# Kernel tuning notes

Measured on AMD Instinct MI355X. Metric: run time of the kernel, lower is better.

Reference implementation:

```python
import jax, jax.numpy as jnp
import numpy as np
from jax import lax

B, T, D, K = 2, 4096, 128, 256


def setup_inputs() -> dict:
    key = jax.random.key(0)
    ks = jax.random.split(key, 5)
    s = 0.05
    return {
        "z": jax.random.normal(ks[0], (B, T, D), jnp.float32),
        "conv_kernel": jax.random.normal(ks[1], (K, 1, D), jnp.float32) * s,  # flax WIO depthwise
        "conv_bias": jnp.zeros((D,), jnp.float32),
        "Wq": jax.random.normal(ks[2], (D, D), jnp.float32) * s,
        "bq": jnp.zeros((D,), jnp.float32),
        "Wk": jax.random.normal(ks[3], (D, D), jnp.float32) * s,
        "bk": jnp.zeros((D,), jnp.float32),
        "Wo": jax.random.normal(ks[4], (D, D), jnp.float32) * s,
        "bo": jnp.zeros((D,), jnp.float32),
    }


def _sphere_norm(x):
    return x / jnp.maximum(jnp.linalg.norm(x, axis=-1, keepdims=True), 1e-8)


def reference(z, conv_kernel, conv_bias, Wq, bq, Wk, bk, Wo, bo):
    Bv, Tv, Dv = z.shape
    Kv = conv_kernel.shape[0]

    # Depthwise causal memory conv (flax nn.Conv, padding='CAUSAL', groups=D)
    memory_force = lax.conv_general_dilated(
        z, conv_kernel, window_strides=(1,), padding=[(Kv - 1, 0)],
        dimension_numbers=("NWC", "WIO", "NWC"), feature_group_count=Dv,
    ) + conv_bias

    # Keys are computed from the base point z once, shared across RK4 stages
    k_hat = _sphere_norm(z @ Wk + bk)  # [B,T,D]
    mask = jnp.tril(jnp.ones((Tv, Tv), z.dtype))  # causal mask

    def vector_field(z_curr):
        q_hat = _sphere_norm(z_curr @ Wq + bq)
        dots = jnp.einsum("btd,bsd->bts", q_hat, k_hat)  # [B,T,T]
        attn = jnp.sin(dots) * mask  # Kuramoto-style sin coupling, causal
        kuramoto = jnp.einsum("bts,bsd->btd", attn, k_hat) @ Wo + bo
        total = memory_force + kuramoto
        # project to tangent space of the sphere at z_curr
        return total - jnp.sum(total * z_curr, axis=-1, keepdims=True) * z_curr

    h = 1.0

    def retract(z_base, v):
        return _sphere_norm(z_base + v)

    k1 = vector_field(z)
    k2 = vector_field(retract(z, 0.5 * h * k1))
    k3 = vector_field(retract(z, 0.5 * h * k2))
    k4 = vector_field(retract(z, h * k3))
    v_final = (h / 6.0) * (k1 + 2 * k2 + 2 * k3 + k4)
    return retract(z, v_final)
```

## Files before the change

kernel.cpp:

```cpp
#include <hip/hip_runtime.h>
#include <hip/hip_bf16.h>

#define BB 2
#define TT 4096
#define DD 128
#define KK 256
#define NROW (BB*TT)
#define NELT (NROW*DD)

typedef _Float16 f16;
typedef __attribute__((ext_vector_type(8))) f16 half8;
typedef __attribute__((ext_vector_type(2))) __fp16 fp16x2;
typedef __attribute__((ext_vector_type(4))) float f32x4;
typedef __attribute__((ext_vector_type(2))) int i32x2;

__device__ __forceinline__ int pack2(float a, float b){
  fp16x2 h = __builtin_amdgcn_cvt_pkrtz(a, b);
  return __builtin_bit_cast(int, h);
}

__device__ __forceinline__ void stage_w_f16(int tid, const float* __restrict__ W, f16* Wh){
  #pragma unroll
  for (int it = 0; it < 8; it++){
    int idx = tid + it*256;
    f32x4 a = *(const f32x4*)(W + (size_t)idx*8);
    f32x4 b = *(const f32x4*)(W + (size_t)idx*8 + 4);
    half8 h;
    #pragma unroll
    for (int u = 0; u < 4; u++){ h[u] = (f16)a[u]; h[4+u] = (f16)b[u]; }
    *(half8*)(Wh + (size_t)idx*8) = h;
  }
}

__device__ __forceinline__ void proj_norm_rows(
    int tid, int r0,
    const float* __restrict__ src, const float* __restrict__ W, const float* __restrict__ bias,
    f16* __restrict__ dst, f16* __restrict__ dstT)
{
  __shared__ f16 Wh[DD*DD];
  __shared__ float zs[32*DD];
  stage_w_f16(tid, W, Wh);
  #pragma unroll
  for (int it = 0; it < 4; it++){
    int idx = tid + it*256;
    *(f32x4*)(zs + idx*4) = *(const f32x4*)(src + (size_t)r0*DD + idx*4);
  }
  __syncthreads();
  int c = tid & 15, rr = tid >> 4;
  float acc0[8], acc1[8];
  #pragma unroll
  for (int u = 0; u < 8; u++){ float bv = bias[c*8+u]; acc0[u] = bv; acc1[u] = bv; }
  const float* zr0 = zs + rr*DD;
  const float* zr1 = zs + (rr+16)*DD;
  #pragma unroll 4
  for (int i = 0; i < DD; i++){
    half8 wv = *(const half8*)(Wh + i*DD + c*8);
    float a0 = zr0[i], a1 = zr1[i];
    #pragma unroll
    for (int u = 0; u < 8; u++){
      float w = (float)wv[u];
      acc0[u] = fmaf(a0, w, acc0[u]);
      acc1[u] = fmaf(a1, w, acc1[u]);
    }
  }
  float s0 = 0.f, s1 = 0.f;
  #pragma unroll
  for (int u = 0; u < 8; u++){ s0 = fmaf(acc0[u], acc0[u], s0); s1 = fmaf(acc1[u], acc1[u], s1); }
  #pragma unroll
  for (int m = 1; m < 16; m <<= 1){ s0 += __shfl_xor(s0, m, 16); s1 += __shfl_xor(s1, m, 16); }
  float inv0 = 1.f / fmaxf(sqrtf(s0), 1e-8f);
  float inv1 = 1.f / fmaxf(sqrtf(s1), 1e-8f);
  half8 h0, h1;
  #pragma unroll
  for (int u = 0; u < 8; u++){ h0[u] = (f16)(acc0[u]*inv0); h1[u] = (f16)(acc1[u]*inv1); }
  int row0 = r0 + rr, row1 = row0 + 16;
  *(half8*)(dst + (size_t)row0*DD + c*8) = h0;
  *(half8*)(dst + (size_t)row1*DD + c*8) = h1;
  if (dstT){
    int b = row0 >> 12, t0 = row0 & 4095, t1 = row1 & 4095;
    #pragma unroll
    for (int u = 0; u < 8; u++){
      dstT[((size_t)b*DD + c*8 + u)*TT + t0] = h0[u];
      dstT[((size_t)b*DD + c*8 + u)*TT + t1] = h1[u];
    }
  }
}

__global__ __launch_bounds__(256) void k_prep(
    const float* __restrict__ z, const float* __restrict__ Wk, const float* __restrict__ bk,
    const float* __restrict__ ck, const float* __restrict__ cb,
    const float* __restrict__ Wq, const float* __restrict__ bq,
    f16* __restrict__ khb, f16* __restrict__ khT, f16* __restrict__ qhb,
    float* __restrict__ mf)
{
  int tid = threadIdx.x;
  if (blockIdx.x < 512){
    int bid = blockIdx.x;
    int d = tid & 127, tg = tid >> 7;
    int b = bid >> 8;
    int tbase = ((bid & 255) << 4) + tg*8;
    const float* zb = z + (size_t)b*TT*DD;
    float acc[8];
    #pragma unroll
    for (int j = 0; j < 8; j++) acc[j] = 0.f;
    float ckq[8];
    #pragma unroll
    for (int u = 0; u < 8; u++) ckq[u] = 0.f;
    int sstart = tbase - (KK-1);
    for (int ch = 0; ch < 33; ch++){
      #pragma unroll
      for (int u = 0; u < 8; u++){
        int base = ch*8 + u;
        int s = sstart + base;
        float zv = ((unsigned)s < (unsigned)TT && base < 263) ? zb[(size_t)s*DD + d] : 0.f;
        ckq[u] = (base < KK) ? ck[(size_t)base*DD + d] : 0.f;
        #pragma unroll
        for (int j = 0; j < 8; j++) acc[j] = fmaf(ckq[(u-j)&7], zv, acc[j]);
      }
    }
    float cbv = cb[d];
    #pragma unroll
    for (int j = 0; j < 8; j++)
      mf[((size_t)b*TT + tbase + j)*DD + d] = acc[j] + cbv;
  } else if (blockIdx.x < 768){
    proj_norm_rows(tid, (blockIdx.x - 512) * 32, z, Wk, bk, khb, khT);
  } else {
    proj_norm_rows(tid, (blockIdx.x - 768) * 32, z, Wq, bq, qhb, nullptr);
  }
}

#define QTILE 128
#define NQT3 (TT/QTILE)
#define NCHUNK 272

__global__ __launch_bounds__(256,2) void k_attn13(
    const f16* __restrict__ qhb, const f16* __restrict__ khb,
    const f16* __restrict__ khT, f16* __restrict__ part)
{
  int bid = blockIdx.x;
  int b = bid / NCHUNK;
  int rem = bid - b*NCHUNK;
  int qt = 0, chunk = 0;
  #pragma unroll 1
  for (int j = NQT3-1; j >= 0; j--){
    int nch = (2*j + 5) >> 2;
    if (rem < nch){ qt = j; chunk = rem; break; }
    rem -= nch;
  }
  int kt0 = chunk * 4;
  int kt1 = min(kt0 + 3, 2*qt + 1);
  int t0 = qt * QTILE;

  __shared__ __align__(16) f16 Kb[64*136];
  __shared__ __align__(16) f16 Kt[128*72];
  __shared__ __align__(16) f16 Ps[4][32*72];

  int tid  = threadIdx.x;
  int w    = tid >> 6;
  int lane = tid & 63;
  int n16  = lane & 15;
  int g    = lane >> 4;

  const f16* qg  = qhb + (size_t)b*TT*DD;
  const f16* kg  = khb + (size_t)b*TT*DD;
  const f16* ktg = khT + (size_t)b*DD*TT;

  int sb_r  = tid >> 4, sb_c = (tid & 15)*8;
  int st_r  = tid >> 3, st_c = (tid & 7)*8;

  half8 qa[2][4];
  #pragma unroll
  for (int p = 0; p < 2; p++){
    const f16* qrow = qg + (size_t)(t0 + 32*w + 16*p + n16)*DD + g*8;
    #pragma unroll
    for (int c = 0; c < 4; c++) qa[p][c] = *(const half8*)(qrow + 32*c);
  }
  f32x4 acc[2][8];
  #pragma unroll
  for (int p = 0; p < 2; p++)
    #pragma unroll
    for (int i = 0; i < 8; i++) acc[p][i] = (f32x4){0.f,0.f,0.f,0.f};

  f16* psw = &Ps[w][0];

  half8 sKb[4], sKt[4];
  {
    int s0 = kt0 * 64;
    #pragma unroll
    for (int it = 0; it < 4; it++)
      sKb[it] = *(const half8*)(kg + (size_t)(s0 + sb_r + it*16)*DD + sb_c);
    #pragma unroll
    for (int it = 0; it < 4; it++)
      sKt[it] = *(const half8*)(ktg + (size_t)(st_r + it*32)*TT + s0 + st_c);
  }

  for (int kt = kt0; kt <= kt1; kt++){
    #pragma unroll
    for (int it = 0; it < 4; it++)
      *(half8*)(Kb + (sb_r + it*16)*136 + sb_c) = sKb[it];
    #pragma unroll
    for (int it = 0; it < 4; it++)
      *(half8*)(Kt + (st_r + it*32)*72 + st_c) = sKt[it];
    __syncthreads();

    if (kt < kt1){
      int s0n = (kt+1) * 64;
      #pragma unroll
      for (int it = 0; it < 4; it++)
        sKb[it] = *(const half8*)(kg + (size_t)(s0n + sb_r + it*16)*DD + sb_c);
      #pragma unroll
      for (int it = 0; it < 4; it++)
        sKt[it] = *(const half8*)(ktg + (size_t)(st_r + it*32)*TT + s0n + st_c);
    }

    int s0 = kt * 64;
    f32x4 s_acc[2][4];
    #pragma unroll
    for (int p = 0; p < 2; p++)
      #pragma unroll
      for (int n = 0; n < 4; n++) s_acc[p][n] = (f32x4){0.f,0.f,0.f,0.f};
    #pragma unroll
    for (int c = 0; c < 4; c++){
      #pragma unroll
      for (int n = 0; n < 4; n++){
        half8 af = *(const half8*)(Kb + (16*n + n16)*136 + 32*c + g*8);
        s_acc[0][n] = __builtin_amdgcn_mfma_f32_16x16x32_f16(af, qa[0][c], s_acc[0][n], 0,0,0);
        s_acc[1][n] = __builtin_amdgcn_mfma_f32_16x16x32_f16(af, qa[1][c], s_acc[1][n], 0,0,0);
      }
    }
    #pragma unroll
    for (int p = 0; p < 2; p++){
      int qrow = t0 + 32*w + 16*p + n16;
      #pragma unroll
      for (int n = 0; n < 4; n++){
        int keyr = s0 + 16*n + 4*g;
        float v0 = (keyr     <= qrow) ? __sinf(s_acc[p][n][0]) : 0.f;
        float v1 = (keyr + 1 <= qrow) ? __sinf(s_acc[p][n][1]) : 0.f;
        float v2 = (keyr + 2 <= qrow) ? __sinf(s_acc[p][n][2]) : 0.f;
        float v3 = (keyr + 3 <= qrow) ? __sinf(s_acc[p][n][3]) : 0.f;
        i32x2 pw = { pack2(v0, v1), pack2(v2, v3) };
        *(i32x2*)(psw + (16*p + n16)*72 + 16*n + 4*g) = pw;
      }
    }

    #pragma unroll
    for (int h = 0; h < 2; h++){
      half8 pa[2];
      #pragma unroll
      for (int p = 0; p < 2; p++)
        pa[p] = *(const half8*)(psw + (16*p + n16)*72 + 32*h + 8*g);
      #pragma unroll
      for (int nt = 0; nt < 8; nt++){
        half8 bf = *(const half8*)(Kt + (16*nt + n16)*72 + 32*h + 8*g);
        acc[0][nt] = __builtin_amdgcn_mfma_f32_16x16x32_f16(pa[0], bf, acc[0][nt], 0,0,0);
        acc[1][nt] = __builtin_amdgcn_mfma_f32_16x16x32_f16(pa[1], bf, acc[1][nt], 0,0,0);
      }
    }
    __syncthreads();
  }

  f16* pb = part + (size_t)bid*(QTILE*DD) + (32*w)*DD;
  #pragma unroll
  for (int p = 0; p < 2; p++){
    #pragma unroll
    for (int nt = 0; nt < 8; nt++){
      #pragma unroll
      for (int r = 0; r < 4; r++){
        pb[(size_t)(16*p + 4*g + r)*DD + 16*nt + n16] = (f16)acc[p][nt][r];
      }
    }
  }
}

__global__ __launch_bounds__(256,2) void k_comb2(
    const float* __restrict__ z, const float* __restrict__ Wo, const float* __restrict__ bo,
    const float* __restrict__ mf, const f16* __restrict__ part,
    const float* __restrict__ zin, float* __restrict__ zout,
    float* __restrict__ vsum, float* __restrict__ out,
    const float* __restrict__ Wq, const float* __restrict__ bq, f16* __restrict__ qhb,
    float wsum, float cretr, int first, int last)
{
  __shared__ f16 Wh[DD*DD];
  __shared__ f16 Wqh[DD*DD];
  __shared__ float As[16*DD];
  int tid = threadIdx.x;
  int r0 = blockIdx.x * 16;
  stage_w_f16(tid, Wo, Wh);
  if (!last) stage_w_f16(tid, Wq, Wqh);
  {
    int b = r0 >> 12;
    int t = r0 & 4095;
    int qt = t >> 7;
    int ro = t & 127;
    int nc = (2*qt + 5) >> 2;
    int base = 0;
    #pragma unroll 1
    for (int j = NQT3-1; j > qt; j--) base += (2*j + 5) >> 2;
    size_t sb = ((size_t)b*NCHUNK + base)*(QTILE*DD) + (size_t)ro*DD;
    const f16* s = part + sb + (size_t)tid*8;
    float a[8];
    {
      half8 v = *(const half8*)(s);
      #pragma unroll
      for (int u = 0; u < 8; u++) a[u] = (float)v[u];
    }
    for (int cc = 1; cc < nc; cc++){
      half8 v = *(const half8*)(s + (size_t)cc*(QTILE*DD));
      #pragma unroll
      for (int u = 0; u < 8; u++) a[u] += (float)v[u];
    }
    f32x4 o0v = {a[0],a[1],a[2],a[3]}, o1v = {a[4],a[5],a[6],a[7]};
    *(f32x4*)(As + (size_t)tid*8) = o0v;
    *(f32x4*)(As + (size_t)tid*8 + 4) = o1v;
  }
  __syncthreads();
  int c = tid & 15, rr = tid >> 4;
  float kur0[8];
  #pragma unroll
  for (int u = 0; u < 8; u++){ kur0[u] = bo[c*8+u]; }
  const float* ar0 = As + rr*DD;
  #pragma unroll 4
  for (int i = 0; i < DD; i++){
    half8 wv = *(const half8*)(Wh + i*DD + c*8);
    float a0 = ar0[i];
    #pragma unroll
    for (int u = 0; u < 8; u++){
      kur0[u] = fmaf(a0, (float)wv[u], kur0[u]);
    }
  }
  size_t o0 = (size_t)(r0+rr)*DD + c*8;
  float tot0[8], zi0[8];
  {
    f32x4 m0a = *(const f32x4*)(mf + o0), m0b = *(const f32x4*)(mf + o0 + 4);
    f32x4 z0a = *(const f32x4*)(zin + o0), z0b = *(const f32x4*)(zin + o0 + 4);
    #pragma unroll
    for (int u = 0; u < 4; u++){
      tot0[u] = m0a[u] + kur0[u]; tot0[4+u] = m0b[u] + kur0[4+u];
      zi0[u] = z0a[u]; zi0[4+u] = z0b[u];
    }
  }
  float p0 = 0.f;
  #pragma unroll
  for (int u = 0; u < 8; u++){ p0 = fmaf(tot0[u], zi0[u], p0); }
  #pragma unroll
  for (int m = 1; m < 16; m <<= 1){ p0 += __shfl_xor(p0, m, 16); }
  float ki0[8], vs0[8];
  #pragma unroll
  for (int u = 0; u < 8; u++){
    ki0[u] = tot0[u] - p0 * zi0[u];
  }
  if (first){
    #pragma unroll
    for (int u = 0; u < 8; u++){ vs0[u] = wsum*ki0[u]; }
  } else {
    f32x4 v0a = *(const f32x4*)(vsum + o0), v0b = *(const f32x4*)(vsum + o0 + 4);
    #pragma unroll
    for (int u = 0; u < 4; u++){
      vs0[u] = fmaf(wsum, ki0[u], v0a[u]); vs0[4+u] = fmaf(wsum, ki0[4+u], v0b[u]);
    }
  }
  if (!last){
    f32x4 va = {vs0[0],vs0[1],vs0[2],vs0[3]}, vb = {vs0[4],vs0[5],vs0[6],vs0[7]};
    *(f32x4*)(vsum + o0) = va; *(f32x4*)(vsum + o0 + 4) = vb;
  }
  float nz0[8];
  {
    f32x4 z0a = *(const f32x4*)(z + o0), z0b = *(const f32x4*)(z + o0 + 4);
    #pragma unroll
    for (int u = 0; u < 4; u++){
      float d0a = last ? vs0[u]*(1.f/6.f)   : cretr*ki0[u];
      float d0b = last ? vs0[4+u]*(1.f/6.f) : cretr*ki0[4+u];
      nz0[u] = z0a[u] + d0a; nz0[4+u] = z0b[u] + d0b;
    }
  }
  float n0 = 0.f;
  #pragma unroll
  for (int u = 0; u < 8; u++){ n0 = fmaf(nz0[u], nz0[u], n0); }
  #pragma unroll
  for (int m = 1; m < 16; m <<= 1){ n0 += __shfl_xor(n0, m, 16); }
  float i0 = 1.f / fmaxf(sqrtf(n0), 1e-8f);
  float* dst = last ? out : zout;
  f32x4 ra = {nz0[0]*i0, nz0[1]*i0, nz0[2]*i0, nz0[3]*i0};
  f32x4 rb = {nz0[4]*i0, nz0[5]*i0, nz0[6]*i0, nz0[7]*i0};
  *(f32x4*)(dst + o0) = ra; *(f32x4*)(dst + o0 + 4) = rb;

  if (!last){
    __syncthreads();
    *(f32x4*)(As + rr*DD + c*8)          = ra;
    *(f32x4*)(As + rr*DD + c*8 + 4)      = rb;
    __syncthreads();
    float q0[8];
    #pragma unroll
    for (int u = 0; u < 8; u++){ q0[u] = bq[c*8+u]; }
    const float* qr0 = As + rr*DD;
    #pragma unroll 4
    for (int i = 0; i < DD; i++){
      half8 wv = *(const half8*)(Wqh + i*DD + c*8);
      float a0 = qr0[i];
      #pragma unroll
      for (int u = 0; u < 8; u++){
        q0[u] = fmaf(a0, (float)wv[u], q0[u]);
      }
    }
    float s0 = 0.f;
    #pragma unroll
    for (int u = 0; u < 8; u++){ s0 = fmaf(q0[u], q0[u], s0); }
    #pragma unroll
    for (int m = 1; m < 16; m <<= 1){ s0 += __shfl_xor(s0, m, 16); }
    float qi0 = 1.f / fmaxf(sqrtf(s0), 1e-8f);
    half8 h0;
    #pragma unroll
    for (int u = 0; u < 8; u++){ h0[u] = (f16)(q0[u]*qi0); }
    *(half8*)(qhb + (size_t)(r0+rr)*DD + c*8) = h0;
  }
}

extern "C" void kernel_launch(void* const* d_in, const int* in_sizes, int n_in,
                              void* d_out, int out_size, void* d_ws, size_t ws_size,
                              hipStream_t stream) {
  const float* z  = (const float*)d_in[0];
  const float* ck = (const float*)d_in[1];
  const float* cb = (const float*)d_in[2];
  const float* Wq = (const float*)d_in[3];
  const float* bq = (const float*)d_in[4];
  const float* Wk = (const float*)d_in[5];
  const float* bk = (const float*)d_in[6];
  const float* Wo = (const float*)d_in[7];
  const float* bo = (const float*)d_in[8];
  float* out = (float*)d_out;

  float* mf   = (float*)d_ws;
  float* zc   = mf   + NELT;
  float* vsum = zc   + NELT;
  f16*   khb  = (f16*)(vsum + NELT);
  f16*   khT  = khb  + NELT;
  f16*   qhb  = khT  + NELT;
  f16*   part = qhb  + NELT;

  k_prep<<<1024, 256, 0, stream>>>(z, Wk, bk, ck, cb, Wq, bq, khb, khT, qhb, mf);

  const float wv[4] = {1.f, 2.f, 2.f, 1.f};
  const float cv[4] = {0.5f, 0.5f, 1.f, 0.f};
  for (int st = 0; st < 4; st++){
    const float* zcur = (st == 0) ? z : zc;
    k_attn13<<<BB*NCHUNK, 256, 0, stream>>>(qhb, khb, khT, part);
    k_comb2 <<<NROW/16, 256, 0, stream>>>(z, Wo, bo, mf, part, zcur, zc, vsum, out,
                                          Wq, bq, qhb, wv[st], cv[st], st == 0, st == 3);
  }
}
```

Before: 286.0 us.

## Fuse attention and combine into one kernel with a grid-wide atomic barrier

Merges the per-stage attention kernel and the combine/Wo/Wq-projection kernel into a single persistent kernel. Blocks spin on a per-stage atomic counter, zeroed in the prep kernel, as a grid barrier between the two phases. Shared memory for both phases is overlaid through a union. The key-chunk size per block grows from 4 to 10 tiles, so the attention grid shrinks to 238 blocks, and the combine phase grid-strides over the row groups. This removes one launch per RK4 stage and the idle tail between kernels. In exchange it accepts fewer attention blocks, and it depends on all blocks being resident at once, or the barrier deadlocks.

```diff
diff --git a/kernel.cpp b/kernel.cpp
--- a/kernel.cpp
+++ b/kernel.cpp
@@ -91,9 +91,10 @@
     const float* __restrict__ ck, const float* __restrict__ cb,
     const float* __restrict__ Wq, const float* __restrict__ bq,
     f16* __restrict__ khb, f16* __restrict__ khT, f16* __restrict__ qhb,
-    float* __restrict__ mf)
+    float* __restrict__ mf, int* __restrict__ ctr)
 {
   int tid = threadIdx.x;
+  if (blockIdx.x == 0 && tid < 8) ctr[tid] = 0;
   if (blockIdx.x < 512){
     int bid = blockIdx.x;
     int d = tid & 127, tg = tid >> 7;
@@ -131,287 +132,302 @@
 
 #define QTILE 128
 #define NQT3 (TT/QTILE)
-#define NCHUNK 272
-
-__global__ __launch_bounds__(256,2) void k_attn13(
-    const f16* __restrict__ qhb, const f16* __restrict__ khb,
-    const f16* __restrict__ khT, f16* __restrict__ part)
-{
-  int bid = blockIdx.x;
-  int b = bid / NCHUNK;
-  int rem = bid - b*NCHUNK;
-  int qt = 0, chunk = 0;
-  #pragma unroll 1
-  for (int j = NQT3-1; j >= 0; j--){
-    int nch = (2*j + 5) >> 2;
-    if (rem < nch){ qt = j; chunk = rem; break; }
-    rem -= nch;
-  }
-  int kt0 = chunk * 4;
-  int kt1 = min(kt0 + 3, 2*qt + 1);
-  int t0 = qt * QTILE;
-
-  __shared__ __align__(16) f16 Kb[64*136];
-  __shared__ __align__(16) f16 Kt[128*72];
-  __shared__ __align__(16) f16 Ps[4][32*72];
-
-  int tid  = threadIdx.x;
-  int w    = tid >> 6;
-  int lane = tid & 63;
-  int n16  = lane & 15;
-  int g    = lane >> 4;
-
-  const f16* qg  = qhb + (size_t)b*TT*DD;
-  const f16* kg  = khb + (size_t)b*TT*DD;
-  const f16* ktg = khT + (size_t)b*DD*TT;
-
-  int sb_r  = tid >> 4, sb_c = (tid & 15)*8;
-  int st_r  = tid >> 3, st_c = (tid & 7)*8;
-
-  half8 qa[2][4];
-  #pragma unroll
-  for (int p = 0; p < 2; p++){
-    const f16* qrow = qg + (size_t)(t0 + 32*w + 16*p + n16)*DD + g*8;
-    #pragma unroll
-    for (int c = 0; c < 4; c++) qa[p][c] = *(const half8*)(qrow + 32*c);
-  }
-  f32x4 acc[2][8];
-  #pragma unroll
-  for (int p = 0; p < 2; p++)
-    #pragma unroll
-    for (int i = 0; i < 8; i++) acc[p][i] = (f32x4){0.f,0.f,0.f,0.f};
-
-  f16* psw = &Ps[w][0];
-
-  half8 sKb[4], sKt[4];
-  {
-    int s0 = kt0 * 64;
-    #pragma unroll
-    for (int it = 0; it < 4; it++)
-      sKb[it] = *(const half8*)(kg + (size_t)(s0 + sb_r + it*16)*DD + sb_c);
-    #pragma unroll
-    for (int it = 0; it < 4; it++)
-      sKt[it] = *(const half8*)(ktg + (size_t)(st_r + it*32)*TT + s0 + st_c);
-  }
-
-  for (int kt = kt0; kt <= kt1; kt++){
-    #pragma unroll
-    for (int it = 0; it < 4; it++)
-      *(half8*)(Kb + (sb_r + it*16)*136 + sb_c) = sKb[it];
-    #pragma unroll
-    for (int it = 0; it < 4; it++)
-      *(half8*)(Kt + (st_r + it*32)*72 + st_c) = sKt[it];
-    __syncthreads();
-
-    if (kt < kt1){
-      int s0n = (kt+1) * 64;
-      #pragma unroll
-      for (int it = 0; it < 4; it++)
-        sKb[it] = *(const half8*)(kg + (size_t)(s0n + sb_r + it*16)*DD + sb_c);
-      #pragma unroll
-      for (int it = 0; it < 4; it++)
-        sKt[it] = *(const half8*)(ktg + (size_t)(st_r + it*32)*TT + s0n + st_c);
-    }
-
-    int s0 = kt * 64;
-    f32x4 s_acc[2][4];
-    #pragma unroll
-    for (int p = 0; p < 2; p++)
-      #pragma unroll
-      for (int n = 0; n < 4; n++) s_acc[p][n] = (f32x4){0.f,0.f,0.f,0.f};
-    #pragma unroll
-    for (int c = 0; c < 4; c++){
-      #pragma unroll
-      for (int n = 0; n < 4; n++){
-        half8 af = *(const half8*)(Kb + (16*n + n16)*136 + 32*c + g*8);
-        s_acc[0][n] = __builtin_amdgcn_mfma_f32_16x16x32_f16(af, qa[0][c], s_acc[0][n], 0,0,0);
-        s_acc[1][n] = __builtin_amdgcn_mfma_f32_16x16x32_f16(af, qa[1][c], s_acc[1][n], 0,0,0);
-      }
-    }
-    #pragma unroll
-    for (int p = 0; p < 2; p++){
-      int qrow = t0 + 32*w + 16*p + n16;
-      #pragma unroll
-      for (int n = 0; n < 4; n++){
-        int keyr = s0 + 16*n + 4*g;
-        float v0 = (keyr     <= qrow) ? __sinf(s_acc[p][n][0]) : 0.f;
-        float v1 = (keyr + 1 <= qrow) ? __sinf(s_acc[p][n][1]) : 0.f;
-        float v2 = (keyr + 2 <= qrow) ? __sinf(s_acc[p][n][2]) : 0.f;
-        float v3 = (keyr + 3 <= qrow) ? __sinf(s_acc[p][n][3]) : 0.f;
-        i32x2 pw = { pack2(v0, v1), pack2(v2, v3) };
-        *(i32x2*)(psw + (16*p + n16)*72 + 16*n + 4*g) = pw;
-      }
-    }
-
-    #pragma unroll
-    for (int h = 0; h < 2; h++){
-      half8 pa[2];
-      #pragma unroll
-      for (int p = 0; p < 2; p++)
-        pa[p] = *(const half8*)(psw + (16*p + n16)*72 + 32*h + 8*g);
-      #pragma unroll
-      for (int nt = 0; nt < 8; nt++){
-        half8 bf = *(const half8*)(Kt + (16*nt + n16)*72 + 32*h + 8*g);
-        acc[0][nt] = __builtin_amdgcn_mfma_f32_16x16x32_f16(pa[0], bf, acc[0][nt], 0,0,0);
-        acc[1][nt] = __builtin_amdgcn_mfma_f32_16x16x32_f16(pa[1], bf, acc[1][nt], 0,0,0);
-      }
-    }
-    __syncthreads();
-  }
-
-  f16* pb = part + (size_t)bid*(QTILE*DD) + (32*w)*DD;
-  #pragma unroll
-  for (int p = 0; p < 2; p++){
-    #pragma unroll
-    for (int nt = 0; nt < 8; nt++){
-      #pragma unroll
-      for (int r = 0; r < 4; r++){
-        pb[(size_t)(16*p + 4*g + r)*DD + 16*nt + n16] = (f16)acc[p][nt][r];
-      }
-    }
-  }
-}
-
-__global__ __launch_bounds__(256,2) void k_comb2(
+#define CH 10
+#define NCHUNK 119
+#define NBLK (BB*NCHUNK)
+
+union __align__(16) SU {
+  struct { f16 Kb[64*136]; f16 Kt[128*72]; f16 Ps[4][32*72]; } a;
+  struct { f16 Wh[DD*DD];  f16 Wqh[DD*DD]; float As[16*DD]; } c;
+};
+
+__global__ __launch_bounds__(256) void k_stage(
+    f16* __restrict__ qhb, const f16* __restrict__ khb,
+    const f16* __restrict__ khT, f16* __restrict__ part,
     const float* __restrict__ z, const float* __restrict__ Wo, const float* __restrict__ bo,
-    const float* __restrict__ mf, const f16* __restrict__ part,
-    const float* __restrict__ zin, float* __restrict__ zout,
+    const float* __restrict__ mf, const float* __restrict__ zin, float* __restrict__ zout,
     float* __restrict__ vsum, float* __restrict__ out,
-    const float* __restrict__ Wq, const float* __restrict__ bq, f16* __restrict__ qhb,
+    const float* __restrict__ Wq, const float* __restrict__ bq,
+    int* __restrict__ ctr,
     float wsum, float cretr, int first, int last)
 {
-  __shared__ f16 Wh[DD*DD];
-  __shared__ f16 Wqh[DD*DD];
-  __shared__ float As[16*DD];
-  int tid = threadIdx.x;
-  int r0 = blockIdx.x * 16;
-  stage_w_f16(tid, Wo, Wh);
-  if (!last) stage_w_f16(tid, Wq, Wqh);
+  __shared__ SU S;
+  int tid  = threadIdx.x;
+  int bid  = blockIdx.x;
+
   {
-    int b = r0 >> 12;
-    int t = r0 & 4095;
-    int qt = t >> 7;
-    int ro = t & 127;
-    int nc = (2*qt + 5) >> 2;
-    int base = 0;
+    int b = bid / NCHUNK;
+    int rem = bid - b*NCHUNK;
+    int qt = 0, chunk = 0;
     #pragma unroll 1
-    for (int j = NQT3-1; j > qt; j--) base += (2*j + 5) >> 2;
-    size_t sb = ((size_t)b*NCHUNK + base)*(QTILE*DD) + (size_t)ro*DD;
-    const f16* s = part + sb + (size_t)tid*8;
-    float a[8];
+    for (int j = NQT3-1; j >= 0; j--){
+      int nch = (2*j + 11) / CH;
+      if (rem < nch){ qt = j; chunk = rem; break; }
+      rem -= nch;
+    }
+    int kt0 = chunk * CH;
+    int kt1 = min(kt0 + CH-1, 2*qt + 1);
+    int t0 = qt * QTILE;
+
+    int w    = tid >> 6;
+    int lane = tid & 63;
+    int n16  = lane & 15;
+    int g    = lane >> 4;
+
+    const f16* qg  = qhb + (size_t)b*TT*DD;
+    const f16* kg  = khb + (size_t)b*TT*DD;
+    const f16* ktg = khT + (size_t)b*DD*TT;
+
+    int sb_r  = tid >> 4, sb_c = (tid & 15)*8;
+    int st_r  = tid >> 3, st_c = (tid & 7)*8;
+
+    half8 qa[2][4];
+    #pragma unroll
+    for (int p = 0; p < 2; p++){
+      const f16* qrow = qg + (size_t)(t0 + 32*w + 16*p + n16)*DD + g*8;
+      #pragma unroll
+      for (int c = 0; c < 4; c++) qa[p][c] = *(const half8*)(qrow + 32*c);
+    }
+    f32x4 acc[2][8];
+    #pragma unroll
+    for (int p = 0; p < 2; p++)
+      #pragma unroll
+      for (int i = 0; i < 8; i++) acc[p][i] = (f32x4){0.f,0.f,0.f,0.f};
+
+    f16* psw = &S.a.Ps[w][0];
+
+    half8 sKb[4], sKt[4];
     {
-      half8 v = *(const half8*)(s);
-      #pragma unroll
-      for (int u = 0; u < 8; u++) a[u] = (float)v[u];
-    }
-    for (int cc = 1; cc < nc; cc++){
-      half8 v = *(const half8*)(s + (size_t)cc*(QTILE*DD));
-      #pragma unroll
-      for (int u = 0; u < 8; u++) a[u] += (float)v[u];
-    }
-    f32x4 o0v = {a[0],a[1],a[2],a[3]}, o1v = {a[4],a[5],a[6],a[7]};
-    *(f32x4*)(As + (size_t)tid*8) = o0v;
-    *(f32x4*)(As + (size_t)tid*8 + 4) = o1v;
-  }
+      int s0 = kt0 * 64;
+      #pragma unroll
+      for (int it = 0; it < 4; it++)
+        sKb[it] = *(const half8*)(kg + (size_t)(s0 + sb_r + it*16)*DD + sb_c);
+      #pragma unroll
+      for (int it = 0; it < 4; it++)
+        sKt[it] = *(const half8*)(ktg + (size_t)(st_r + it*32)*TT + s0 + st_c);
+    }
+
+    for (int kt = kt0; kt <= kt1; kt++){
+      #pragma unroll
+      for (int it = 0; it < 4; it++)
+        *(half8*)(S.a.Kb + (sb_r + it*16)*136 + sb_c) = sKb[it];
+      #pragma unroll
+      for (int it = 0; it < 4; it++)
+        *(half8*)(S.a.Kt + (st_r + it*32)*72 + st_c) = sKt[it];
+      __syncthreads();
+
+      if (kt < kt1){
+        int s0n = (kt+1) * 64;
+        #pragma unroll
+        for (int it = 0; it < 4; it++)
+          sKb[it] = *(const half8*)(kg + (size_t)(s0n + sb_r + it*16)*DD + sb_c);
+        #pragma unroll
+        for (int it = 0; it < 4; it++)
+          sKt[it] = *(const half8*)(ktg + (size_t)(st_r + it*32)*TT + s0n + st_c);
+      }
+
+      int s0 = kt * 64;
+      f32x4 s_acc[2][4];
+      #pragma unroll
+      for (int p = 0; p < 2; p++)
+        #pragma unroll
+        for (int n = 0; n < 4; n++) s_acc[p][n] = (f32x4){0.f,0.f,0.f,0.f};
+      #pragma unroll
+      for (int c = 0; c < 4; c++){
+        #pragma unroll
+        for (int n = 0; n < 4; n++){
+          half8 af = *(const half8*)(S.a.Kb + (16*n + n16)*136 + 32*c + g*8);
+          s_acc[0][n] = __builtin_amdgcn_mfma_f32_16x16x32_f16(af, qa[0][c], s_acc[0][n], 0,0,0);
+          s_acc[1][n] = __builtin_amdgcn_mfma_f32_16x16x32_f16(af, qa[1][c], s_acc[1][n], 0,0,0);
+        }
+      }
+      #pragma unroll
+      for (int p = 0; p < 2; p++){
+        int qrow = t0 + 32*w + 16*p + n16;
+        #pragma unroll
+        for (int n = 0; n < 4; n++){
+          int keyr = s0 + 16*n + 4*g;
+          float v0 = (keyr     <= qrow) ? __sinf(s_acc[p][n][0]) : 0.f;
+          float v1 = (keyr + 1 <= qrow) ? __sinf(s_acc[p][n][1]) : 0.f;
+          float v2 = (keyr + 2 <= qrow) ? __sinf(s_acc[p][n][2]) : 0.f;
+          float v3 = (keyr + 3 <= qrow) ? __sinf(s_acc[p][n][3]) : 0.f;
+          i32x2 pw = { pack2(v0, v1), pack2(v2, v3) };
+          *(i32x2*)(psw + (16*p + n16)*72 + 16*n + 4*g) = pw;
+        }
+      }
+      #pragma unroll
+      for (int h = 0; h < 2; h++){
+        half8 pa[2];
+        #pragma unroll
+        for (int p = 0; p < 2; p++)
+          pa[p] = *(const half8*)(psw + (16*p + n16)*72 + 32*h + 8*g);
+        #pragma unroll
+        for (int nt = 0; nt < 8; nt++){
+          half8 bf = *(const half8*)(S.a.Kt + (16*nt + n16)*72 + 32*h + 8*g);
+          acc[0][nt] = __builtin_amdgcn_mfma_f32_16x16x32_f16(pa[0], bf, acc[0][nt], 0,0,0);
+          acc[1][nt] = __builtin_amdgcn_mfma_f32_16x16x32_f16(pa[1], bf, acc[1][nt], 0,0,0);
+        }
+      }
+      __syncthreads();
+    }
+
+    f16* pb = part + (size_t)bid*(QTILE*DD) + (32*w)*DD;
+    #pragma unroll
+    for (int p = 0; p < 2; p++){
+      #pragma unroll
+      for (int nt = 0; nt < 8; nt++){
+        #pragma unroll
+        for (int r = 0; r < 4; r++){
+          pb[(size_t)(16*p + 4*g + r)*DD + 16*nt + n16] = (f16)acc[p][nt][r];
+        }
+      }
+    }
+  }
+
   __syncthreads();
-  int c = tid & 15, rr = tid >> 4;
-  float kur0[8];
-  #pragma unroll
-  for (int u = 0; u < 8; u++){ kur0[u] = bo[c*8+u]; }
-  const float* ar0 = As + rr*DD;
-  #pragma unroll 4
-  for (int i = 0; i < DD; i++){
-    half8 wv = *(const half8*)(Wh + i*DD + c*8);
-    float a0 = ar0[i];
-    #pragma unroll
-    for (int u = 0; u < 8; u++){
-      kur0[u] = fmaf(a0, (float)wv[u], kur0[u]);
-    }
-  }
-  size_t o0 = (size_t)(r0+rr)*DD + c*8;
-  float tot0[8], zi0[8];
+  if (tid == 0){
+    __threadfence();
+    __hip_atomic_fetch_add(ctr, 1, __ATOMIC_RELEASE, __HIP_MEMORY_SCOPE_AGENT);
+    while (__hip_atomic_load(ctr, __ATOMIC_ACQUIRE, __HIP_MEMORY_SCOPE_AGENT) < NBLK)
+      __builtin_amdgcn_s_sleep(2);
+  }
+  __syncthreads();
+
   {
-    f32x4 m0a = *(const f32x4*)(mf + o0), m0b = *(const f32x4*)(mf + o0 + 4);
-    f32x4 z0a = *(const f32x4*)(zin + o0), z0b = *(const f32x4*)(zin + o0 + 4);
-    #pragma unroll
-    for (int u = 0; u < 4; u++){
-      tot0[u] = m0a[u] + kur0[u]; tot0[4+u] = m0b[u] + kur0[4+u];
-      zi0[u] = z0a[u]; zi0[4+u] = z0b[u];
-    }
-  }
-  float p0 = 0.f;
-  #pragma unroll
-  for (int u = 0; u < 8; u++){ p0 = fmaf(tot0[u], zi0[u], p0); }
-  #pragma unroll
-  for (int m = 1; m < 16; m <<= 1){ p0 += __shfl_xor(p0, m, 16); }
-  float ki0[8], vs0[8];
-  #pragma unroll
-  for (int u = 0; u < 8; u++){
-    ki0[u] = tot0[u] - p0 * zi0[u];
-  }
-  if (first){
-    #pragma unroll
-    for (int u = 0; u < 8; u++){ vs0[u] = wsum*ki0[u]; }
-  } else {
-    f32x4 v0a = *(const f32x4*)(vsum + o0), v0b = *(const f32x4*)(vsum + o0 + 4);
-    #pragma unroll
-    for (int u = 0; u < 4; u++){
-      vs0[u] = fmaf(wsum, ki0[u], v0a[u]); vs0[4+u] = fmaf(wsum, ki0[4+u], v0b[u]);
-    }
-  }
-  if (!last){
-    f32x4 va = {vs0[0],vs0[1],vs0[2],vs0[3]}, vb = {vs0[4],vs0[5],vs0[6],vs0[7]};
-    *(f32x4*)(vsum + o0) = va; *(f32x4*)(vsum + o0 + 4) = vb;
-  }
-  float nz0[8];
-  {
-    f32x4 z0a = *(const f32x4*)(z + o0), z0b = *(const f32x4*)(z + o0 + 4);
-    #pragma unroll
-    for (int u = 0; u < 4; u++){
-      float d0a = last ? vs0[u]*(1.f/6.f)   : cretr*ki0[u];
-      float d0b = last ? vs0[4+u]*(1.f/6.f) : cretr*ki0[4+u];
-      nz0[u] = z0a[u] + d0a; nz0[4+u] = z0b[u] + d0b;
-    }
-  }
-  float n0 = 0.f;
-  #pragma unroll
-  for (int u = 0; u < 8; u++){ n0 = fmaf(nz0[u], nz0[u], n0); }
-  #pragma unroll
-  for (int m = 1; m < 16; m <<= 1){ n0 += __shfl_xor(n0, m, 16); }
-  float i0 = 1.f / fmaxf(sqrtf(n0), 1e-8f);
-  float* dst = last ? out : zout;
-  f32x4 ra = {nz0[0]*i0, nz0[1]*i0, nz0[2]*i0, nz0[3]*i0};
-  f32x4 rb = {nz0[4]*i0, nz0[5]*i0, nz0[6]*i0, nz0[7]*i0};
-  *(f32x4*)(dst + o0) = ra; *(f32x4*)(dst + o0 + 4) = rb;
-
-  if (!last){
-    __syncthreads();
-    *(f32x4*)(As + rr*DD + c*8)          = ra;
-    *(f32x4*)(As + rr*DD + c*8 + 4)      = rb;
-    __syncthreads();
-    float q0[8];
-    #pragma unroll
-    for (int u = 0; u < 8; u++){ q0[u] = bq[c*8+u]; }
-    const float* qr0 = As + rr*DD;
-    #pragma unroll 4
-    for (int i = 0; i < DD; i++){
-      half8 wv = *(const half8*)(Wqh + i*DD + c*8);
-      float a0 = qr0[i];
+    f16* Wh = S.c.Wh; f16* Wqh = S.c.Wqh; float* As = S.c.As;
+    stage_w_f16(tid, Wo, Wh);
+    if (!last) stage_w_f16(tid, Wq, Wqh);
+    #pragma unroll 1
+    for (int gq = bid; gq < NROW/16; gq += NBLK){
+      __syncthreads();
+      int r0 = gq * 16;
+      {
+        int b = r0 >> 12;
+        int t = r0 & 4095;
+        int qt = t >> 7;
+        int ro = t & 127;
+        int nc = (2*qt + 11) / CH;
+        int base = 0;
+        #pragma unroll 1
+        for (int j = NQT3-1; j > qt; j--) base += (2*j + 11) / CH;
+        size_t sb = ((size_t)b*NCHUNK + base)*(QTILE*DD) + (size_t)ro*DD;
+        const f16* s = part + sb + (size_t)tid*8;
+        float a[8];
+        {
+          half8 v = *(const half8*)(s);
+          #pragma unroll
+          for (int u = 0; u < 8; u++) a[u] = (float)v[u];
+        }
+        for (int cc = 1; cc < nc; cc++){
+          half8 v = *(const half8*)(s + (size_t)cc*(QTILE*DD));
+          #pragma unroll
+          for (int u = 0; u < 8; u++) a[u] += (float)v[u];
+        }
+        f32x4 o0v = {a[0],a[1],a[2],a[3]}, o1v = {a[4],a[5],a[6],a[7]};
+        *(f32x4*)(As + (size_t)tid*8) = o0v;
+        *(f32x4*)(As + (size_t)tid*8 + 4) = o1v;
+      }
+      __syncthreads();
+      int c = tid & 15, rr = tid >> 4;
+      float kur0[8];
+      #pragma unroll
+      for (int u = 0; u < 8; u++){ kur0[u] = bo[c*8+u]; }
+      const float* ar0 = As + rr*DD;
+      #pragma unroll 4
+      for (int i = 0; i < DD; i++){
+        half8 wv = *(const half8*)(Wh + i*DD + c*8);
+        float a0 = ar0[i];
+        #pragma unroll
+        for (int u = 0; u < 8; u++){
+          kur0[u] = fmaf(a0, (float)wv[u], kur0[u]);
+        }
+      }
+      size_t o0 = (size_t)(r0+rr)*DD + c*8;
+      float tot0[8], zi0[8];
+      {
+        f32x4 m0a = *(const f32x4*)(mf + o0), m0b = *(const f32x4*)(mf + o0 + 4);
+        f32x4 z0a = *(const f32x4*)(zin + o0), z0b = *(const f32x4*)(zin + o0 + 4);
+        #pragma unroll
+        for (int u = 0; u < 4; u++){
+          tot0[u] = m0a[u] + kur0[u]; tot0[4+u] = m0b[u] + kur0[4+u];
+          zi0[u] = z0a[u]; zi0[4+u] = z0b[u];
+        }
+      }
+      float p0 = 0.f;
+      #pragma unroll
+      for (int u = 0; u < 8; u++){ p0 = fmaf(tot0[u], zi0[u], p0); }
+      #pragma unroll
+      for (int m = 1; m < 16; m <<= 1){ p0 += __shfl_xor(p0, m, 16); }
+      float ki0[8], vs0[8];
       #pragma unroll
       for (int u = 0; u < 8; u++){
-        q0[u] = fmaf(a0, (float)wv[u], q0[u]);
-      }
-    }
-    float s0 = 0.f;
-    #pragma unroll
-    for (int u = 0; u < 8; u++){ s0 = fmaf(q0[u], q0[u], s0); }
-    #pragma unroll
-    for (int m = 1; m < 16; m <<= 1){ s0 += __shfl_xor(s0, m, 16); }
-    float qi0 = 1.f / fmaxf(sqrtf(s0), 1e-8f);
-    half8 h0;
-    #pragma unroll
-    for (int u = 0; u < 8; u++){ h0[u] = (f16)(q0[u]*qi0); }
-    *(half8*)(qhb + (size_t)(r0+rr)*DD + c*8) = h0;
+        ki0[u] = tot0[u] - p0 * zi0[u];
+      }
+      if (first){
+        #pragma unroll
+        for (int u = 0; u < 8; u++){ vs0[u] = wsum*ki0[u]; }
+      } else {
+        f32x4 v0a = *(const f32x4*)(vsum + o0), v0b = *(const f32x4*)(vsum + o0 + 4);
+        #pragma unroll
+        for (int u = 0; u < 4; u++){
+          vs0[u] = fmaf(wsum, ki0[u], v0a[u]); vs0[4+u] = fmaf(wsum, ki0[4+u], v0b[u]);
+        }
+      }
+      if (!last){
+        f32x4 va = {vs0[0],vs0[1],vs0[2],vs0[3]}, vb = {vs0[4],vs0[5],vs0[6],vs0[7]};
+        *(f32x4*)(vsum + o0) = va; *(f32x4*)(vsum + o0 + 4) = vb;
+      }
+      float nz0[8];
+      {
+        f32x4 z0a = *(const f32x4*)(z + o0), z0b = *(const f32x4*)(z + o0 + 4);
+        #pragma unroll
+        for (int u = 0; u < 4; u++){
+          float d0a = last ? vs0[u]*(1.f/6.f)   : cretr*ki0[u];
+          float d0b = last ? vs0[4+u]*(1.f/6.f) : cretr*ki0[4+u];
+          nz0[u] = z0a[u] + d0a; nz0[4+u] = z0b[u] + d0b;
+        }
+      }
+      float n0 = 0.f;
+      #pragma unroll
+      for (int u = 0; u < 8; u++){ n0 = fmaf(nz0[u], nz0[u], n0); }
+      #pragma unroll
+      for (int m = 1; m < 16; m <<= 1){ n0 += __shfl_xor(n0, m, 16); }
+      float i0 = 1.f / fmaxf(sqrtf(n0), 1e-8f);
+      float* dst = last ? out : zout;
+      f32x4 ra = {nz0[0]*i0, nz0[1]*i0, nz0[2]*i0, nz0[3]*i0};
+      f32x4 rb = {nz0[4]*i0, nz0[5]*i0, nz0[6]*i0, nz0[7]*i0};
+      *(f32x4*)(dst + o0) = ra; *(f32x4*)(dst + o0 + 4) = rb;
+
+      if (!last){
+        __syncthreads();
+        *(f32x4*)(As + rr*DD + c*8)     = ra;
+        *(f32x4*)(As + rr*DD + c*8 + 4) = rb;
+        __syncthreads();
+        float q0[8];
+        #pragma unroll
+        for (int u = 0; u < 8; u++){ q0[u] = bq[c*8+u]; }
+        const float* qr0 = As + rr*DD;
+        #pragma unroll 4
+        for (int i = 0; i < DD; i++){
+          half8 wv = *(const half8*)(Wqh + i*DD + c*8);
+          float a0 = qr0[i];
+          #pragma unroll
+          for (int u = 0; u < 8; u++){
+            q0[u] = fmaf(a0, (float)wv[u], q0[u]);
+          }
+        }
+        float s0 = 0.f;
+        #pragma unroll
+        for (int u = 0; u < 8; u++){ s0 = fmaf(q0[u], q0[u], s0); }
+        #pragma unroll
+        for (int m = 1; m < 16; m <<= 1){ s0 += __shfl_xor(s0, m, 16); }
+        float qi0 = 1.f / fmaxf(sqrtf(s0), 1e-8f);
+        half8 h0;
+        #pragma unroll
+        for (int u = 0; u < 8; u++){ h0[u] = (f16)(q0[u]*qi0); }
+        *(half8*)(qhb + (size_t)(r0+rr)*DD + c*8) = h0;
+      }
+    }
   }
 }
 
@@ -436,15 +452,16 @@
   f16*   khT  = khb  + NELT;
   f16*   qhb  = khT  + NELT;
   f16*   part = qhb  + NELT;
-
-  k_prep<<<1024, 256, 0, stream>>>(z, Wk, bk, ck, cb, Wq, bq, khb, khT, qhb, mf);
+  int*   ctr  = (int*)(part + (size_t)NBLK*QTILE*DD);
+
+  k_prep<<<1024, 256, 0, stream>>>(z, Wk, bk, ck, cb, Wq, bq, khb, khT, qhb, mf, ctr);
 
   const float wv[4] = {1.f, 2.f, 2.f, 1.f};
   const float cv[4] = {0.5f, 0.5f, 1.f, 0.f};
   for (int st = 0; st < 4; st++){
     const float* zcur = (st == 0) ? z : zc;
-    k_attn13<<<BB*NCHUNK, 256, 0, stream>>>(qhb, khb, khT, part);
-    k_comb2 <<<NROW/16, 256, 0, stream>>>(z, Wo, bo, mf, part, zcur, zc, vsum, out,
-                                          Wq, bq, qhb, wv[st], cv[st], st == 0, st == 3);
-  }
-}
+    k_stage<<<NBLK, 256, 0, stream>>>(qhb, khb, khT, part, z, Wo, bo, mf, zcur, zc,
+                                      vsum, out, Wq, bq, ctr + st,
+                                      wv[st], cv[st], st == 0, st == 3);
+  }
+}
```

Result: slower. 474.7 us (+66.0%).

## Rewrite attention kernel with 32x32 MFMA and register-resident K fragments, no LDS

Applied to the files above, without the earlier changes.

The attention kernel now uses 32x32x16 MFMA tiles instead of 16x16x32. Each wave loads its K and K-transpose fragments straight from global memory into registers, which removes the shared-memory staging, the P scratch buffer and the block barriers. The sin-coupling scores are repacked into A-operand layout with cross-half-wave shuffles rather than a round trip through LDS. In exchange, every wave reloads the same K tiles from global or L2 memory, the global-to-register prefetch is gone, and register pressure rises.

```diff
diff --git a/kernel.cpp b/kernel.cpp
--- a/kernel.cpp
+++ b/kernel.cpp
@@ -12,7 +12,9 @@
 typedef __attribute__((ext_vector_type(8))) f16 half8;
 typedef __attribute__((ext_vector_type(2))) __fp16 fp16x2;
 typedef __attribute__((ext_vector_type(4))) float f32x4;
+typedef __attribute__((ext_vector_type(16))) float f32x16;
 typedef __attribute__((ext_vector_type(2))) int i32x2;
+typedef __attribute__((ext_vector_type(4))) int i32x4;
 
 __device__ __forceinline__ int pack2(float a, float b){
   fp16x2 h = __builtin_amdgcn_cvt_pkrtz(a, b);
@@ -133,7 +135,7 @@
 #define NQT3 (TT/QTILE)
 #define NCHUNK 272
 
-__global__ __launch_bounds__(256,2) void k_attn13(
+__global__ __launch_bounds__(256,2) void k_attn16(
     const f16* __restrict__ qhb, const f16* __restrict__ khb,
     const f16* __restrict__ khT, f16* __restrict__ part)
 {
@@ -151,123 +153,108 @@
   int kt1 = min(kt0 + 3, 2*qt + 1);
   int t0 = qt * QTILE;
 
-  __shared__ __align__(16) f16 Kb[64*136];
-  __shared__ __align__(16) f16 Kt[128*72];
-  __shared__ __align__(16) f16 Ps[4][32*72];
-
   int tid  = threadIdx.x;
   int w    = tid >> 6;
   int lane = tid & 63;
-  int n16  = lane & 15;
-  int g    = lane >> 4;
+  int q31  = lane & 31;
+  int hi   = lane >> 5;
 
   const f16* qg  = qhb + (size_t)b*TT*DD;
   const f16* kg  = khb + (size_t)b*TT*DD;
   const f16* ktg = khT + (size_t)b*DD*TT;
 
-  int sb_r  = tid >> 4, sb_c = (tid & 15)*8;
-  int st_r  = tid >> 3, st_c = (tid & 7)*8;
-
-  half8 qa[2][4];
-  #pragma unroll
-  for (int p = 0; p < 2; p++){
-    const f16* qrow = qg + (size_t)(t0 + 32*w + 16*p + n16)*DD + g*8;
-    #pragma unroll
-    for (int c = 0; c < 4; c++) qa[p][c] = *(const half8*)(qrow + 32*c);
-  }
-  f32x4 acc[2][8];
-  #pragma unroll
-  for (int p = 0; p < 2; p++)
-    #pragma unroll
-    for (int i = 0; i < 8; i++) acc[p][i] = (f32x4){0.f,0.f,0.f,0.f};
-
-  f16* psw = &Ps[w][0];
-
-  half8 sKb[4], sKt[4];
+  int qrow_g = t0 + 32*w + q31;
+
+  half8 qb[8];
   {
-    int s0 = kt0 * 64;
-    #pragma unroll
-    for (int it = 0; it < 4; it++)
-      sKb[it] = *(const half8*)(kg + (size_t)(s0 + sb_r + it*16)*DD + sb_c);
-    #pragma unroll
-    for (int it = 0; it < 4; it++)
-      sKt[it] = *(const half8*)(ktg + (size_t)(st_r + it*32)*TT + s0 + st_c);
-  }
-
+    const f16* qrow = qg + (size_t)qrow_g*DD + 8*hi;
+    #pragma unroll
+    for (int ks = 0; ks < 8; ks++) qb[ks] = *(const half8*)(qrow + 16*ks);
+  }
+
+  f32x16 acc[4];
+  #pragma unroll
+  for (int d = 0; d < 4; d++)
+    #pragma unroll
+    for (int i = 0; i < 16; i++) acc[d][i] = 0.f;
+
+  #pragma unroll 1
   for (int kt = kt0; kt <= kt1; kt++){
-    #pragma unroll
-    for (int it = 0; it < 4; it++)
-      *(half8*)(Kb + (sb_r + it*16)*136 + sb_c) = sKb[it];
-    #pragma unroll
-    for (int it = 0; it < 4; it++)
-      *(half8*)(Kt + (st_r + it*32)*72 + st_c) = sKt[it];
-    __syncthreads();
-
-    if (kt < kt1){
-      int s0n = (kt+1) * 64;
-      #pragma unroll
-      for (int it = 0; it < 4; it++)
-        sKb[it] = *(const half8*)(kg + (size_t)(s0n + sb_r + it*16)*DD + sb_c);
-      #pragma unroll
-      for (int it = 0; it < 4; it++)
-        sKt[it] = *(const half8*)(ktg + (size_t)(st_r + it*32)*TT + s0n + st_c);
-    }
-
     int s0 = kt * 64;
-    f32x4 s_acc[2][4];
-    #pragma unroll
-    for (int p = 0; p < 2; p++)
-      #pragma unroll
-      for (int n = 0; n < 4; n++) s_acc[p][n] = (f32x4){0.f,0.f,0.f,0.f};
-    #pragma unroll
-    for (int c = 0; c < 4; c++){
-      #pragma unroll
-      for (int n = 0; n < 4; n++){
-        half8 af = *(const half8*)(Kb + (16*n + n16)*136 + 32*c + g*8);
-        s_acc[0][n] = __builtin_amdgcn_mfma_f32_16x16x32_f16(af, qa[0][c], s_acc[0][n], 0,0,0);
-        s_acc[1][n] = __builtin_amdgcn_mfma_f32_16x16x32_f16(af, qa[1][c], s_acc[1][n], 0,0,0);
+
+    half8 kf[2][8];
+    #pragma unroll
+    for (int kb = 0; kb < 2; kb++){
+      const f16* krow = kg + (size_t)(s0 + 32*kb + q31)*DD + 8*hi;
+      #pragma unroll
+      for (int ks = 0; ks < 8; ks++) kf[kb][ks] = *(const half8*)(krow + 16*ks);
+    }
+    f32x16 sa0, sa1;
+    #pragma unroll
+    for (int i = 0; i < 16; i++){ sa0[i] = 0.f; sa1[i] = 0.f; }
+    #pragma unroll
+    for (int ks = 0; ks < 8; ks++){
+      sa0 = __builtin_amdgcn_mfma_f32_32x32x16_f16(kf[0][ks], qb[ks], sa0, 0,0,0);
+      sa1 = __builtin_amdgcn_mfma_f32_32x32x16_f16(kf[1][ks], qb[ks], sa1, 0,0,0);
+    }
+
+    half8 ktf[4][4];
+    #pragma unroll
+    for (int d0 = 0; d0 < 4; d0++){
+      const f16* ktrow = ktg + (size_t)(32*d0 + q31)*TT + s0 + 8*hi;
+      #pragma unroll
+      for (int s = 0; s < 4; s++) ktf[d0][s] = *(const half8*)(ktrow + 16*s);
+    }
+
+    float p0v[16], p1v[16];
+    #pragma unroll
+    for (int r = 0; r < 16; r++){
+      int kr = (r&3) + 8*(r>>2) + 4*hi;
+      int key0 = s0 + kr;
+      int key1 = s0 + 32 + kr;
+      p0v[r] = (key0 <= qrow_g) ? __sinf(sa0[r]) : 0.f;
+      p1v[r] = (key1 <= qrow_g) ? __sinf(sa1[r]) : 0.f;
+    }
+
+    half8 pf[4];
+    #pragma unroll
+    for (int kb = 0; kb < 2; kb++){
+      const float* pv = kb ? p1v : p0v;
+      #pragma unroll
+      for (int u = 0; u < 2; u++){
+        int pl0 = pack2(pv[8*u+0], pv[8*u+1]);
+        int pl1 = pack2(pv[8*u+2], pv[8*u+3]);
+        int ph0 = pack2(pv[8*u+4], pv[8*u+5]);
+        int ph1 = pack2(pv[8*u+6], pv[8*u+7]);
+        int xl0 = __shfl_xor(pl0, 32);
+        int xl1 = __shfl_xor(pl1, 32);
+        int xh0 = __shfl_xor(ph0, 32);
+        int xh1 = __shfl_xor(ph1, 32);
+        i32x4 fr;
+        fr[0] = hi ? xh0 : pl0;
+        fr[1] = hi ? xh1 : pl1;
+        fr[2] = hi ? ph0 : xl0;
+        fr[3] = hi ? ph1 : xl1;
+        pf[2*kb+u] = __builtin_bit_cast(half8, fr);
       }
     }
-    #pragma unroll
-    for (int p = 0; p < 2; p++){
-      int qrow = t0 + 32*w + 16*p + n16;
-      #pragma unroll
-      for (int n = 0; n < 4; n++){
-        int keyr = s0 + 16*n + 4*g;
-        float v0 = (keyr     <= qrow) ? __sinf(s_acc[p][n][0]) : 0.f;
-        float v1 = (keyr + 1 <= qrow) ? __sinf(s_acc[p][n][1]) : 0.f;
-        float v2 = (keyr + 2 <= qrow) ? __sinf(s_acc[p][n][2]) : 0.f;
-        float v3 = (keyr + 3 <= qrow) ? __sinf(s_acc[p][n][3]) : 0.f;
-        i32x2 pw = { pack2(v0, v1), pack2(v2, v3) };
-        *(i32x2*)(psw + (16*p + n16)*72 + 16*n + 4*g) = pw;
+
+    #pragma unroll
+    for (int s = 0; s < 4; s++){
+      #pragma unroll
+      for (int d0 = 0; d0 < 4; d0++){
+        acc[d0] = __builtin_amdgcn_mfma_f32_32x32x16_f16(pf[s], ktf[d0][s], acc[d0], 0,0,0);
       }
     }
-
-    #pragma unroll
-    for (int h = 0; h < 2; h++){
-      half8 pa[2];
-      #pragma unroll
-      for (int p = 0; p < 2; p++)
-        pa[p] = *(const half8*)(psw + (16*p + n16)*72 + 32*h + 8*g);
-      #pragma unroll
-      for (int nt = 0; nt < 8; nt++){
-        half8 bf = *(const half8*)(Kt + (16*nt + n16)*72 + 32*h + 8*g);
-        acc[0][nt] = __builtin_amdgcn_mfma_f32_16x16x32_f16(pa[0], bf, acc[0][nt], 0,0,0);
-        acc[1][nt] = __builtin_amdgcn_mfma_f32_16x16x32_f16(pa[1], bf, acc[1][nt], 0,0,0);
-      }
-    }
-    __syncthreads();
-  }
-
-  f16* pb = part + (size_t)bid*(QTILE*DD) + (32*w)*DD;
-  #pragma unroll
-  for (int p = 0; p < 2; p++){
-    #pragma unroll
-    for (int nt = 0; nt < 8; nt++){
-      #pragma unroll
-      for (int r = 0; r < 4; r++){
-        pb[(size_t)(16*p + 4*g + r)*DD + 16*nt + n16] = (f16)acc[p][nt][r];
-      }
+  }
+
+  f16* pb = part + (size_t)bid*(QTILE*DD);
+  #pragma unroll
+  for (int d0 = 0; d0 < 4; d0++){
+    #pragma unroll
+    for (int r = 0; r < 16; r++){
+      int qr = 32*w + (r&3) + 8*(r>>2) + 4*hi;
+      pb[(size_t)qr*DD + 32*d0 + q31] = (f16)acc[d0][r];
     }
   }
 }
@@ -386,8 +373,8 @@
 
   if (!last){
     __syncthreads();
-    *(f32x4*)(As + rr*DD + c*8)          = ra;
-    *(f32x4*)(As + rr*DD + c*8 + 4)      = rb;
+    *(f32x4*)(As + rr*DD + c*8)     = ra;
+    *(f32x4*)(As + rr*DD + c*8 + 4) = rb;
     __syncthreads();
     float q0[8];
     #pragma unroll
@@ -443,7 +430,7 @@
   const float cv[4] = {0.5f, 0.5f, 1.f, 0.f};
   for (int st = 0; st < 4; st++){
     const float* zcur = (st == 0) ? z : zc;
-    k_attn13<<<BB*NCHUNK, 256, 0, stream>>>(qhb, khb, khT, part);
+    k_attn16<<<BB*NCHUNK, 256, 0, stream>>>(qhb, khb, khT, part);
     k_comb2 <<<NROW/16, 256, 0, stream>>>(z, Wo, bo, mf, part, zcur, zc, vsum, out,
                                           Wq, bq, qhb, wv[st], cv[st], st == 0, st == 3);
   }
```

Measured after the change: 395.2 us. +38.2%, slower.
